# Optimization experiments

Hardware: AMD Instinct MI355X
Metric: run time of the kernel (lower is better)

## Reference

```python
import jax, jax.numpy as jnp
import numpy as np

B = 4194304  # number of sequential rows


def setup_inputs() -> dict:
    key = jax.random.key(0)
    k1, k2, k3, k4 = jax.random.split(key, 4)
    x = jax.random.normal(k1, (B, 1, 3), dtype=jnp.float32)
    # nn.Linear(3, 3) params
    lim = 1.0 / np.sqrt(3.0)
    W = jax.random.uniform(k2, (3, 3), minval=-lim, maxval=lim, dtype=jnp.float32)
    b = jax.random.uniform(k3, (3,), minval=-lim, maxval=lim, dtype=jnp.float32)
    # FastNetwork init: (-1-1)*rand([3,1]) + 1  -> uniform in [-1, 1]
    net0 = jax.random.uniform(k4, (3, 1), minval=-1.0, maxval=1.0, dtype=jnp.float32)
    return {"x": x, "W": W, "b": b, "net0": net0}


def reference(x, W, b, net0):
    # x: [B,1,3]; W: [3,3]; b: [3]; net0: [3,1]
    xi = x[:, 0, :]                      # [B,3]
    # Updater: per-row Linear(3,3) -- batched as one matmul
    updates = xi @ W.T + b               # [B,3]

    def step(net, inp):
        x_row, u = inp                   # x_row: [3], u: [3]
        # 1/(1+exp(-10*(net + update - 0.5))) == sigmoid(10*(net + update - 0.5))
        net = jax.nn.sigmoid(10.0 * (net + u[:, None] - 0.5))  # [3,1]
        pred = x_row @ net               # [1]
        return net, pred

    _, preds = jax.lax.scan(step, net0, (xi, updates))
    return preds                         # [B,1]
```

## Files before the change

### kernel.cpp

```cpp
#include <hip/hip_runtime.h>


#if __has_builtin(__builtin_amdgcn_exp2f)
#define EXP2F(v) __builtin_amdgcn_exp2f(v)
#else
#define EXP2F(v) __expf(0.6931471805599453f * (v))
#endif

namespace {
constexpr int   BTOT   = 4194304;
constexpr int   CHUNK  = 32;
constexpr int   BLOCK  = 256;
constexpr int   BSTEPS = BLOCK * CHUNK;
constexpr int   WARM   = 32;
constexpr int   GRID   = BTOT / BSTEPS;
constexpr float KEXP   = -14.426950408889634f;
constexpr float EPS    = 1e-5f;
}

#define CVALS(X0_, X1_, X2_)                                                   \
  const float c0 = fmaf(kw00, (X0_), fmaf(kw01, (X1_), fmaf(kw02, (X2_), kb0))); \
  const float c1 = fmaf(kw10, (X0_), fmaf(kw11, (X1_), fmaf(kw12, (X2_), kb1))); \
  const float c2 = fmaf(kw20, (X0_), fmaf(kw21, (X1_), fmaf(kw22, (X2_), kb2)));

#define SIG(N, C) __builtin_amdgcn_rcpf(1.0f + EXP2F(fmaf(KEXP, (N), (C))))

#define PULL(VAL_) \
  __int_as_float(__builtin_amdgcn_ds_bpermute(a1, __float_as_int(VAL_)))

#define FETCH1(S_, XD0, XD1, XD2)                                              \
  XD0 = PULL(fx[3 * (S_) + 0]);                                                \
  XD1 = PULL(fx[3 * (S_) + 1]);                                                \
  XD2 = PULL(fx[3 * (S_) + 2]);                                                \
  if (lane == 0) {                                                             \
    const float4 wv_ = wbuf[w][(S_)];                                          \
    XD0 = wv_.x; XD1 = wv_.y; XD2 = wv_.z;                                     \
  }

#define DSTEP(X0_, X1_, X2_)                                                   \
  {                                                                            \
    CVALS(X0_, X1_, X2_)                                                       \
    lo0 = SIG(lo0, c0); hi0 = SIG(hi0, c0);                                    \
    lo1 = SIG(lo1, c1); hi1 = SIG(hi1, c1);                                    \
    lo2 = SIG(lo2, c2); hi2 = SIG(hi2, c2);                                    \
  }

#define SSTEP(X0_, X1_, X2_)                                                   \
  {                                                                            \
    CVALS(X0_, X1_, X2_)                                                       \
    m0 = SIG(m0, c0); m1 = SIG(m1, c1); m2 = SIG(m2, c2);                      \
  }

#define WBATCH(B_)                                                             \
  {                                                                            \
    float X00,X01,X02,X10,X11,X12,X20,X21,X22,X30,X31,X32;                     \
    FETCH1(4*(B_)+0, X00, X01, X02)                                            \
    FETCH1(4*(B_)+1, X10, X11, X12)                                            \
    FETCH1(4*(B_)+2, X20, X21, X22)                                            \
    FETCH1(4*(B_)+3, X30, X31, X32)                                            \
    if (!single) {                                                             \
      DSTEP(X00, X01, X02) DSTEP(X10, X11, X12)                                \
      DSTEP(X20, X21, X22) DSTEP(X30, X31, X32)                                \
      conv = ((hi0 - lo0) < EPS) & ((hi1 - lo1) < EPS) & ((hi2 - lo2) < EPS);  \
      if (__all(conv)) {                                                       \
        m0 = 0.5f * (lo0 + hi0); m1 = 0.5f * (lo1 + hi1);                      \
        m2 = 0.5f * (lo2 + hi2);                                               \
        single = true;                                                         \
      }                                                                        \
    } else {                                                                   \
      SSTEP(X00, X01, X02) SSTEP(X10, X11, X12)                                \
      SSTEP(X20, X21, X22) SSTEP(X30, X31, X32)                                \
    }                                                                          \
  }

#define MS(P_, X0_, X1_, X2_)                                                  \
  {                                                                            \
    CVALS(X0_, X1_, X2_)                                                       \
    m0 = SIG(m0, c0); m1 = SIG(m1, c1); m2 = SIG(m2, c2);                      \
    P_ = fmaf((X0_), m0, fmaf((X1_), m1, (X2_) * m2));                         \
  }

__global__ __launch_bounds__(BLOCK, 2) void Updater_65395172049297_kernel(
    const float* __restrict__ x, const float* __restrict__ W,
    const float* __restrict__ bv, const float* __restrict__ n0v,
    float* __restrict__ out)
{
    __shared__ float4 wbuf[BLOCK / 64][WARM];

    const float kw00 = KEXP * W[0], kw01 = KEXP * W[1], kw02 = KEXP * W[2];
    const float kw10 = KEXP * W[3], kw11 = KEXP * W[4], kw12 = KEXP * W[5];
    const float kw20 = KEXP * W[6], kw21 = KEXP * W[7], kw22 = KEXP * W[8];
    const float kb0 = KEXP * (bv[0] - 0.5f);
    const float kb1 = KEXP * (bv[1] - 0.5f);
    const float kb2 = KEXP * (bv[2] - 0.5f);
    const float n00 = n0v[0], n01 = n0v[1], n02 = n0v[2];

    const int  lane  = threadIdx.x & 63;
    const int  w     = threadIdx.x >> 6;
    const long S     = (long)blockIdx.x * BSTEPS;
    const long start = S + (long)threadIdx.x * CHUNK;
    const int  a1    = ((lane >= 1) ? (lane - 1) : 0) << 2;

    float fx[96];
    {
        const float4* mp = reinterpret_cast<const float4*>(x + 3 * start);
#pragma unroll
        for (int i = 0; i < 24; ++i) {
            const float4 v = mp[i];
            fx[4 * i + 0] = v.x; fx[4 * i + 1] = v.y;
            fx[4 * i + 2] = v.z; fx[4 * i + 3] = v.w;
        }
    }

    {
        const long wbase = S + (long)w * (64 * CHUNK);
        if (lane < WARM) {
            long sstep = wbase - WARM + lane;
            if (sstep < 0) sstep = 0;
            const float* xp = x + 3 * sstep;
            wbuf[w][lane] = make_float4(xp[0], xp[1], xp[2], 0.0f);
        }
    }
    __syncthreads();

    const bool exact   = (start <= (long)WARM);
    const int  smin    = exact ? (int)(WARM - (int)start) : 0;
    const bool special = (blockIdx.x == 0) && (w == 0);

    float lo0, lo1, lo2, hi0, hi1, hi2;
    if (exact) { lo0 = hi0 = n00; lo1 = hi1 = n01; lo2 = hi2 = n02; }
    else       { lo0 = lo1 = lo2 = 0.0f; hi0 = hi1 = hi2 = 1.0f; }

    bool  conv = false, single = false;
    float m0 = n00, m1 = n01, m2 = n02;

    if (special) {
        for (int s = 0; s < WARM; ++s) {
            if (s >= smin) {
                const long as_ = start - WARM + s;
                const float X0 = x[3 * as_], X1 = x[3 * as_ + 1], X2 = x[3 * as_ + 2];
                DSTEP(X0, X1, X2)
            }
        }
        conv = ((hi0 - lo0) < EPS) & ((hi1 - lo1) < EPS) & ((hi2 - lo2) < EPS);
        if (__all(conv)) {
            m0 = 0.5f * (lo0 + hi0); m1 = 0.5f * (lo1 + hi1); m2 = 0.5f * (lo2 + hi2);
            single = true;
        }
    } else {
        WBATCH(0) WBATCH(1) WBATCH(2) WBATCH(3)
        WBATCH(4) WBATCH(5) WBATCH(6) WBATCH(7)
    }

    if (!single) {
        for (int at = 1; at < 10 && !conv; ++at) {
            long wl2 = (long)WARM << (2 * at);
            long bgn = start - wl2;
            bool ex2 = (bgn <= 0);
            if (ex2) bgn = 0;
            if (ex2) { lo0 = hi0 = n00; lo1 = hi1 = n01; lo2 = hi2 = n02; }
            else     { lo0 = lo1 = lo2 = 0.0f; hi0 = hi1 = hi2 = 1.0f; }
            const float4* bp = reinterpret_cast<const float4*>(x + 3 * bgn);
            const long ng = (start - bgn) >> 2;
            for (long q = 0; q < ng; ++q) {
                const float4 A4 = bp[3 * q], B4 = bp[3 * q + 1], C4 = bp[3 * q + 2];
                DSTEP(A4.x, A4.y, A4.z)
                DSTEP(A4.w, B4.x, B4.y)
                DSTEP(B4.z, B4.w, C4.x)
                DSTEP(C4.y, C4.z, C4.w)
            }
            conv = ex2 || (((hi0 - lo0) < EPS) & ((hi1 - lo1) < EPS) &
                           ((hi2 - lo2) < EPS));
        }
        m0 = 0.5f * (lo0 + hi0); m1 = 0.5f * (lo1 + hi1); m2 = 0.5f * (lo2 + hi2);
    }

    float4* op = reinterpret_cast<float4*>(out + start);
#pragma unroll
    for (int q = 0; q < 8; ++q) {
        float p0, p1, p2, p3;
        MS(p0, fx[12 * q + 0], fx[12 * q + 1],  fx[12 * q + 2]);
        MS(p1, fx[12 * q + 3], fx[12 * q + 4],  fx[12 * q + 5]);
        MS(p2, fx[12 * q + 6], fx[12 * q + 7],  fx[12 * q + 8]);
        MS(p3, fx[12 * q + 9], fx[12 * q + 10], fx[12 * q + 11]);
        op[q] = make_float4(p0, p1, p2, p3);
    }
}

extern "C" void kernel_launch(void* const* d_in, const int* in_sizes, int n_in,
                              void* d_out, int out_size, void* d_ws, size_t ws_size,
                              hipStream_t stream) {
    const float* x   = (const float*)d_in[0];
    const float* W   = (const float*)d_in[1];
    const float* bv  = (const float*)d_in[2];
    const float* n0v = (const float*)d_in[3];
    float*       out = (float*)d_out;
    Updater_65395172049297_kernel<<<GRID, BLOCK, 0, stream>>>(x, W, bv, n0v, out);
}
```

Baseline: 99.69 us.

## Double warm-up window to 64 steps and drop block barrier for wave-local buffer

```diff
diff --git a/kernel.cpp b/kernel.cpp
--- a/kernel.cpp
+++ b/kernel.cpp
@@ -12,7 +12,7 @@
 constexpr int   CHUNK  = 32;
 constexpr int   BLOCK  = 256;
 constexpr int   BSTEPS = BLOCK * CHUNK;
-constexpr int   WARM   = 32;
+constexpr int   WARM   = 64;
 constexpr int   GRID   = BTOT / BSTEPS;
 constexpr float KEXP   = -14.426950408889634f;
 constexpr float EPS    = 1e-5f;
@@ -25,16 +25,26 @@
 
 #define SIG(N, C) __builtin_amdgcn_rcpf(1.0f + EXP2F(fmaf(KEXP, (N), (C))))
 
-#define PULL(VAL_) \
-  __int_as_float(__builtin_amdgcn_ds_bpermute(a1, __float_as_int(VAL_)))
+#define PULL(VAL_, AD_) \
+  __int_as_float(__builtin_amdgcn_ds_bpermute((AD_), __float_as_int(VAL_)))
 
 #define FETCH1(S_, XD0, XD1, XD2)                                              \
-  XD0 = PULL(fx[3 * (S_) + 0]);                                                \
-  XD1 = PULL(fx[3 * (S_) + 1]);                                                \
-  XD2 = PULL(fx[3 * (S_) + 2]);                                                \
-  if (lane == 0) {                                                             \
-    const float4 wv_ = wbuf[w][(S_)];                                          \
-    XD0 = wv_.x; XD1 = wv_.y; XD2 = wv_.z;                                     \
+  if ((S_) < 32) {                                                             \
+    XD0 = PULL(fx[3 * (S_) + 0], a2);                                          \
+    XD1 = PULL(fx[3 * (S_) + 1], a2);                                          \
+    XD2 = PULL(fx[3 * (S_) + 2], a2);                                          \
+    if (lane < 2) {                                                            \
+      const float4 wv_ = wb[(S_) + (lane << 5)];                               \
+      XD0 = wv_.x; XD1 = wv_.y; XD2 = wv_.z;                                   \
+    }                                                                          \
+  } else {                                                                     \
+    XD0 = PULL(fx[3 * ((S_) - 32) + 0], a1);                                   \
+    XD1 = PULL(fx[3 * ((S_) - 32) + 1], a1);                                   \
+    XD2 = PULL(fx[3 * ((S_) - 32) + 2], a1);                                   \
+    if (lane < 1) {                                                            \
+      const float4 wv_ = wb[(S_)];                                             \
+      XD0 = wv_.x; XD1 = wv_.y; XD2 = wv_.z;                                   \
+    }                                                                          \
   }
 
 #define DSTEP(X0_, X1_, X2_)                                                   \
@@ -100,6 +110,17 @@
     const long S     = (long)blockIdx.x * BSTEPS;
     const long start = S + (long)threadIdx.x * CHUNK;
     const int  a1    = ((lane >= 1) ? (lane - 1) : 0) << 2;
+    const int  a2    = ((lane >= 2) ? (lane - 2) : 0) << 2;
+    const float4* wb = wbuf[w];
+
+    float4 wv;
+    {
+        const long wbase = S + (long)w * (64 * CHUNK);
+        long sstep = wbase - WARM + lane;
+        if (sstep < 0) sstep = 0;
+        const float* xp = x + 3 * sstep;
+        wv = make_float4(xp[0], xp[1], xp[2], 0.0f);
+    }
 
     float fx[96];
     {
@@ -112,16 +133,7 @@
         }
     }
 
-    {
-        const long wbase = S + (long)w * (64 * CHUNK);
-        if (lane < WARM) {
-            long sstep = wbase - WARM + lane;
-            if (sstep < 0) sstep = 0;
-            const float* xp = x + 3 * sstep;
-            wbuf[w][lane] = make_float4(xp[0], xp[1], xp[2], 0.0f);
-        }
-    }
-    __syncthreads();
+    wbuf[w][lane] = wv;
 
     const bool exact   = (start <= (long)WARM);
     const int  smin    = exact ? (int)(WARM - (int)start) : 0;
@@ -148,8 +160,10 @@
             single = true;
         }
     } else {
-        WBATCH(0) WBATCH(1) WBATCH(2) WBATCH(3)
-        WBATCH(4) WBATCH(5) WBATCH(6) WBATCH(7)
+        WBATCH(0)  WBATCH(1)  WBATCH(2)  WBATCH(3)
+        WBATCH(4)  WBATCH(5)  WBATCH(6)  WBATCH(7)
+        WBATCH(8)  WBATCH(9)  WBATCH(10) WBATCH(11)
+        WBATCH(12) WBATCH(13) WBATCH(14) WBATCH(15)
     }
 
     if (!single) {
```

New measurement: 106.4 us. +6.7%, slower.
